# Kernel tuning notes

Hardware: AMD Instinct MI355X
Metric: run time of the kernel (lower is better)

The kernel has to match this reference:

```python
import jax, jax.numpy as jnp
import numpy as np


def _normalize_mat(AI):
    # symmetric GCN normalization: D^{-1/2} AI D^{-1/2}, safe for zero rows
    deg = jnp.sum(AI, axis=-1)  # [B, N]
    inv_sqrt = jnp.where(deg > 0, jax.lax.rsqrt(jnp.maximum(deg, 1e-12)), 0.0)
    return AI * inv_sqrt[..., :, None] * inv_sqrt[..., None, :]


def setup_inputs() -> dict:
    key = jax.random.key(0)
    kX, kA, kn, kW, kK = jax.random.split(key, 5)
    B, N, F, OUT, KD = 8, 2048, 256, 256, 32
    X = jax.random.normal(kX, (B, N, F), dtype=jnp.float32)
    A = jax.random.uniform(kA, (B, N, N), dtype=jnp.float32)
    A = 0.5 * (A + jnp.swapaxes(A, -1, -2))  # symmetric dense adjacency weights
    n = jax.random.randint(kn, (B,), 1, N + 1).astype(jnp.int32)
    W = jax.random.normal(kW, (F, OUT), dtype=jnp.float32) * (1.0 / np.sqrt(F))
    W_bias = jnp.zeros((OUT,), dtype=jnp.float32)
    K = jax.random.normal(kK, (F, KD), dtype=jnp.float32) * (1.0 / np.sqrt(F))
    K_bias = jnp.zeros((KD,), dtype=jnp.float32)
    return {"X": X, "A": A, "n": n, "W": W, "W_bias": W_bias, "K": K, "K_bias": K_bias}


def reference(X, A, n, W, W_bias, K, K_bias):
    B, N, F = X.shape
    Id = jnp.eye(N, dtype=X.dtype)  # broadcasts over batch
    # K-projection gating: sigmoid(XK @ XK^T) elementwise-masks A
    XK = jnp.einsum('bnf,fk->bnk', X, K) + K_bias  # [B, N, k_dim]
    A_filter = jax.nn.sigmoid(jnp.einsum('bik,bjk->bij', XK, XK))
    AI = A * A_filter + Id
    AI = _normalize_mat(AI)
    XW = jnp.einsum('bnf,fo->bno', X, W) + W_bias  # [B, N, out_dim]
    XWA = jnp.einsum('bij,bjo->bio', AI, XW)
    X_out = jax.nn.relu(XWA)
    return (X_out, A, n)
```

## Files before the change

kernel.cpp:

```cpp
#include <hip/hip_runtime.h>
#include <cstdint>
#include <cstddef>

#define Bz 8
#define Nn 2048
#define Ff 256
#define OUTD 256
#define KD 32

typedef __attribute__((ext_vector_type(8))) short bf16x8;
typedef __attribute__((ext_vector_type(4))) float f32x4;
typedef unsigned short ushort_t;

__device__ __forceinline__ ushort_t f2bf(float f) {
  union { float f; unsigned int u; } v; v.f = f;
  unsigned int r = v.u + 0x7FFFu + ((v.u >> 16) & 1u);
  return (ushort_t)(r >> 16);
}

__global__ __launch_bounds__(256) void k_xk(const float* __restrict__ X,
                                            const float* __restrict__ K,
                                            const float* __restrict__ Kb,
                                            ushort_t* __restrict__ XKbf) {
  int k = threadIdx.x & 31;
  int rl = threadIdx.x >> 5;
  int row = blockIdx.x * 8 + rl;
  const float* xr = X + (size_t)row * Ff;
  float acc = Kb[k];
#pragma unroll 8
  for (int f = 0; f < Ff; ++f) acc += xr[f] * K[f * KD + k];
  XKbf[(size_t)row * KD + k] = f2bf(acc);
}

__global__ __launch_bounds__(256) void k_degM(const float* __restrict__ A,
                                              const ushort_t* __restrict__ XKbf,
                                              ushort_t* __restrict__ M,
                                              float* __restrict__ deg) {
  int jt = blockIdx.x & 7;
  int it = (blockIdx.x >> 3) & 31;
  int b  = blockIdx.x >> 8;
  int i0 = it * 64, j0 = jt * 256;
  int tid = threadIdx.x;
  int lane = tid & 63, w = tid >> 6;
  int l15 = lane & 15, lh = lane >> 4;

  const ushort_t* XKb = XKbf + (size_t)b * Nn * KD;
  bf16x8 af[4], bfr[4];
#pragma unroll
  for (int m = 0; m < 4; ++m)
    af[m] = *(const bf16x8*)(XKb + (size_t)(i0 + 16 * m + l15) * KD + lh * 8);
#pragma unroll
  for (int n = 0; n < 4; ++n)
    bfr[n] = *(const bf16x8*)(XKb + (size_t)(j0 + 64 * w + 16 * n + l15) * KD + lh * 8);

  f32x4 S[4][4];
#pragma unroll
  for (int m = 0; m < 4; ++m)
#pragma unroll
    for (int n = 0; n < 4; ++n) {
      f32x4 z = {0.f, 0.f, 0.f, 0.f};
      S[m][n] = __builtin_amdgcn_mfma_f32_16x16x32_bf16(af[m], bfr[n], z, 0, 0, 0);
    }

  const float* Ab = A + (size_t)b * Nn * Nn;
  ushort_t* Mb = M + (size_t)b * Nn * Nn;
#pragma unroll
  for (int m = 0; m < 4; ++m) {
#pragma unroll
    for (int r = 0; r < 4; ++r) {
      int row = i0 + 16 * m + lh * 4 + r;
      float ds = 0.f;
#pragma unroll
      for (int n = 0; n < 4; ++n) {
        int col = j0 + 64 * w + 16 * n + l15;
        float d = S[m][n][r];
        float sg = 1.f / (1.f + __expf(-d));
        float mv = Ab[(size_t)row * Nn + col] * sg;
        Mb[(size_t)row * Nn + col] = f2bf(mv);
        ds += mv;
      }
      ds += __shfl_xor(ds, 1, 64);
      ds += __shfl_xor(ds, 2, 64);
      ds += __shfl_xor(ds, 4, 64);
      ds += __shfl_xor(ds, 8, 64);
      if (l15 == 0) atomicAdd(&deg[(size_t)b * Nn + row], ds);
    }
  }
}

__global__ __launch_bounds__(256) void k_xw(const float* __restrict__ X,
                                            const float* __restrict__ W,
                                            const float* __restrict__ Wb,
                                            const float* __restrict__ deg,
                                            float* __restrict__ XWs,
                                            ushort_t* __restrict__ XWsT) {
  __shared__ float Xs[8][Ff];
  int row0 = blockIdx.x * 8;
  int tid = threadIdx.x;
#pragma unroll
  for (int p = 0; p < 2; ++p) {
    int idx = tid + p * 256;
    int r = idx >> 6, c = (idx & 63) * 4;
    *(float4*)&Xs[r][c] = *(const float4*)(X + (size_t)(row0 + r) * Ff + c);
  }
  __syncthreads();
  int o = tid;
  float bias = Wb[o];
  float acc[8];
#pragma unroll
  for (int r = 0; r < 8; ++r) acc[r] = bias;
  for (int f = 0; f < Ff; ++f) {
    float w = W[f * OUTD + o];
#pragma unroll
    for (int r = 0; r < 8; ++r) acc[r] += Xs[r][f] * w;
  }
  int b = row0 / Nn;
  int rl0 = row0 - b * Nn;
  ushort_t mt[8];
#pragma unroll
  for (int r = 0; r < 8; ++r) {
    float is = rsqrtf(1.f + deg[row0 + r]);
    float v = acc[r] * is;
    XWs[(size_t)(row0 + r) * OUTD + o] = v;
    mt[r] = f2bf(v);
  }
  uint4 pk;
  pk.x = (unsigned)mt[0] | ((unsigned)mt[1] << 16);
  pk.y = (unsigned)mt[2] | ((unsigned)mt[3] << 16);
  pk.z = (unsigned)mt[4] | ((unsigned)mt[5] << 16);
  pk.w = (unsigned)mt[6] | ((unsigned)mt[7] << 16);
  *(uint4*)&XWsT[((size_t)b * OUTD + o) * Nn + rl0] = pk;
}

__device__ __forceinline__ void load6(const ushort_t* a0p, const ushort_t* a1p,
                                      const ushort_t* b0p, const ushort_t* b1p,
                                      const ushort_t* b2p, const ushort_t* b3p,
                                      int off,
                                      bf16x8& a0, bf16x8& a1,
                                      bf16x8& b0, bf16x8& b1, bf16x8& b2, bf16x8& b3) {
  a0 = *(const bf16x8*)(a0p + off);
  a1 = *(const bf16x8*)(a1p + off);
  b0 = *(const bf16x8*)(b0p + off);
  b1 = *(const bf16x8*)(b1p + off);
  b2 = *(const bf16x8*)(b2p + off);
  b3 = *(const bf16x8*)(b3p + off);
}

__device__ __forceinline__ void mm8(const bf16x8& a0, const bf16x8& a1,
                                    const bf16x8& b0, const bf16x8& b1,
                                    const bf16x8& b2, const bf16x8& b3,
                                    f32x4 acc[2][4]) {
  acc[0][0] = __builtin_amdgcn_mfma_f32_16x16x32_bf16(a0, b0, acc[0][0], 0, 0, 0);
  acc[0][1] = __builtin_amdgcn_mfma_f32_16x16x32_bf16(a0, b1, acc[0][1], 0, 0, 0);
  acc[0][2] = __builtin_amdgcn_mfma_f32_16x16x32_bf16(a0, b2, acc[0][2], 0, 0, 0);
  acc[0][3] = __builtin_amdgcn_mfma_f32_16x16x32_bf16(a0, b3, acc[0][3], 0, 0, 0);
  acc[1][0] = __builtin_amdgcn_mfma_f32_16x16x32_bf16(a1, b0, acc[1][0], 0, 0, 0);
  acc[1][1] = __builtin_amdgcn_mfma_f32_16x16x32_bf16(a1, b1, acc[1][1], 0, 0, 0);
  acc[1][2] = __builtin_amdgcn_mfma_f32_16x16x32_bf16(a1, b2, acc[1][2], 0, 0, 0);
  acc[1][3] = __builtin_amdgcn_mfma_f32_16x16x32_bf16(a1, b3, acc[1][3], 0, 0, 0);
}

__global__ __launch_bounds__(256) void k_main2(const ushort_t* __restrict__ M,
                                               const ushort_t* __restrict__ XWsT,
                                               const float* __restrict__ XWs,
                                               const float* __restrict__ deg,
                                               float* __restrict__ outX) {
  int it = blockIdx.x & 63;
  int b = blockIdx.x >> 6;
  int i0 = it * 32;
  int tid = threadIdx.x, lane = tid & 63, w = tid >> 6;
  int l15 = lane & 15, lh = lane >> 4;
  const ushort_t* Mb = M + (size_t)b * Nn * Nn;
  const ushort_t* Tb = XWsT + (size_t)b * OUTD * Nn;

  const ushort_t* a0p = Mb + (size_t)(i0 + l15) * Nn + lh * 8;
  const ushort_t* a1p = Mb + (size_t)(i0 + 16 + l15) * Nn + lh * 8;
  const ushort_t* b0p = Tb + (size_t)(64 * w + l15) * Nn + lh * 8;
  const ushort_t* b1p = Tb + (size_t)(64 * w + 16 + l15) * Nn + lh * 8;
  const ushort_t* b2p = Tb + (size_t)(64 * w + 32 + l15) * Nn + lh * 8;
  const ushort_t* b3p = Tb + (size_t)(64 * w + 48 + l15) * Nn + lh * 8;

  f32x4 acc[2][4];
#pragma unroll
  for (int m = 0; m < 2; ++m)
#pragma unroll
    for (int n = 0; n < 4; ++n) acc[m][n] = (f32x4){0.f, 0.f, 0.f, 0.f};

  bf16x8 aA0, aA1, bA0, bA1, bA2, bA3;
  bf16x8 aB0, aB1, bB0, bB1, bB2, bB3;
  bf16x8 aC0, aC1, bC0, bC1, bC2, bC3;
  bf16x8 aD0, aD1, bD0, bD1, bD2, bD3;

  load6(a0p, a1p, b0p, b1p, b2p, b3p, 0 * 32, aA0, aA1, bA0, bA1, bA2, bA3);
  load6(a0p, a1p, b0p, b1p, b2p, b3p, 1 * 32, aB0, aB1, bB0, bB1, bB2, bB3);
  load6(a0p, a1p, b0p, b1p, b2p, b3p, 2 * 32, aC0, aC1, bC0, bC1, bC2, bC3);
  load6(a0p, a1p, b0p, b1p, b2p, b3p, 3 * 32, aD0, aD1, bD0, bD1, bD2, bD3);

  for (int t = 0; t < 64; t += 4) {
    mm8(aA0, aA1, bA0, bA1, bA2, bA3, acc);
    if (t + 4 < 64) load6(a0p, a1p, b0p, b1p, b2p, b3p, (t + 4) * 32, aA0, aA1, bA0, bA1, bA2, bA3);
    mm8(aB0, aB1, bB0, bB1, bB2, bB3, acc);
    if (t + 5 < 64) load6(a0p, a1p, b0p, b1p, b2p, b3p, (t + 5) * 32, aB0, aB1, bB0, bB1, bB2, bB3);
    mm8(aC0, aC1, bC0, bC1, bC2, bC3, acc);
    if (t + 6 < 64) load6(a0p, a1p, b0p, b1p, b2p, b3p, (t + 6) * 32, aC0, aC1, bC0, bC1, bC2, bC3);
    mm8(aD0, aD1, bD0, bD1, bD2, bD3, acc);
    if (t + 7 < 64) load6(a0p, a1p, b0p, b1p, b2p, b3p, (t + 7) * 32, aD0, aD1, bD0, bD1, bD2, bD3);
  }

#pragma unroll
  for (int m = 0; m < 2; ++m) {
#pragma unroll
    for (int r = 0; r < 4; ++r) {
      int row = i0 + 16 * m + lh * 4 + r;
      float is = rsqrtf(1.f + deg[(size_t)b * Nn + row]);
#pragma unroll
      for (int n = 0; n < 4; ++n) {
        int col = 64 * w + 16 * n + l15;
        float v = acc[m][n][r] + XWs[((size_t)b * Nn + row) * OUTD + col];
        outX[((size_t)b * Nn + row) * OUTD + col] = fmaxf(0.f, is * v);
      }
    }
  }
}

__global__ void k_n(const int* __restrict__ n, float* __restrict__ o) {
  if (threadIdx.x < Bz) o[threadIdx.x] = (float)n[threadIdx.x];
}

extern "C" void kernel_launch(void* const* d_in, const int* in_sizes, int n_in,
                              void* d_out, int out_size, void* d_ws, size_t ws_size,
                              hipStream_t stream) {
  const float* X  = (const float*)d_in[0];
  const float* A  = (const float*)d_in[1];
  const int*   nI = (const int*)d_in[2];
  const float* W  = (const float*)d_in[3];
  const float* Wb = (const float*)d_in[4];
  const float* K  = (const float*)d_in[5];
  const float* Kb = (const float*)d_in[6];

  float* outX = (float*)d_out;
  float* outA = outX + (size_t)Bz * Nn * OUTD;
  float* outN = outA + (size_t)Bz * Nn * Nn;

  ushort_t* XKbf = (ushort_t*)d_ws;
  float* deg = (float*)(XKbf + (size_t)Bz * Nn * KD);
  float* XWs = deg + (size_t)Bz * Nn;
  ushort_t* XWsT = (ushort_t*)(XWs + (size_t)Bz * Nn * OUTD);

  ushort_t* Mws = (ushort_t*)outA;

  hipMemsetAsync(deg, 0, (size_t)Bz * Nn * sizeof(float), stream);
  k_xk  <<<dim3(Bz * Nn / 8),  dim3(256), 0, stream>>>(X, K, Kb, XKbf);
  k_degM<<<dim3(Bz * 32 * 8),  dim3(256), 0, stream>>>(A, XKbf, Mws, deg);
  k_xw  <<<dim3(Bz * Nn / 8),  dim3(256), 0, stream>>>(X, W, Wb, deg, XWs, XWsT);
  k_main2<<<dim3(Bz * 64),     dim3(256), 0, stream>>>(Mws, XWsT, XWs, deg, outX);

  hipMemcpyAsync(outA, A, (size_t)Bz * Nn * Nn * sizeof(float),
                 hipMemcpyDeviceToDevice, stream);
  k_n<<<1, 64, 0, stream>>>(nI, outN);
}
```

Before: 484.7 us.

## Fuse A passthrough copy into degM and stage main GEMM tiles through LDS

When the workspace is large enough, the bf16 M matrix goes into the workspace and k_degM writes the fp32 copy of A to the output as it reads it. This removes the separate device-to-device memcpy, which re-read all of A. The main aggregation kernel now stages M and XWsT tiles through double-buffered, XOR-swizzled shared memory, so a block's four waves share loads instead of each wave fetching its own operands from global memory. It also reorders block indices so the batch varies fastest. The fused path depends on ws_size, and the LDS version adds a barrier every k-step.

```diff
diff --git a/kernel.cpp b/kernel.cpp
--- a/kernel.cpp
+++ b/kernel.cpp
@@ -35,7 +35,8 @@
 __global__ __launch_bounds__(256) void k_degM(const float* __restrict__ A,
                                               const ushort_t* __restrict__ XKbf,
                                               ushort_t* __restrict__ M,
-                                              float* __restrict__ deg) {
+                                              float* __restrict__ deg,
+                                              float* __restrict__ Ao) {
   int jt = blockIdx.x & 7;
   int it = (blockIdx.x >> 3) & 31;
   int b  = blockIdx.x >> 8;
@@ -64,6 +65,7 @@
 
   const float* Ab = A + (size_t)b * Nn * Nn;
   ushort_t* Mb = M + (size_t)b * Nn * Nn;
+  float* Aob = Ao ? Ao + (size_t)b * Nn * Nn : nullptr;
 #pragma unroll
   for (int m = 0; m < 4; ++m) {
 #pragma unroll
@@ -73,9 +75,11 @@
 #pragma unroll
       for (int n = 0; n < 4; ++n) {
         int col = j0 + 64 * w + 16 * n + l15;
+        float a = Ab[(size_t)row * Nn + col];
+        if (Aob) Aob[(size_t)row * Nn + col] = a;
         float d = S[m][n][r];
         float sg = 1.f / (1.f + __expf(-d));
-        float mv = Ab[(size_t)row * Nn + col] * sg;
+        float mv = a * sg;
         Mb[(size_t)row * Nn + col] = f2bf(mv);
         ds += mv;
       }
@@ -132,79 +136,75 @@
   *(uint4*)&XWsT[((size_t)b * OUTD + o) * Nn + rl0] = pk;
 }
 
-__device__ __forceinline__ void load6(const ushort_t* a0p, const ushort_t* a1p,
-                                      const ushort_t* b0p, const ushort_t* b1p,
-                                      const ushort_t* b2p, const ushort_t* b3p,
-                                      int off,
-                                      bf16x8& a0, bf16x8& a1,
-                                      bf16x8& b0, bf16x8& b1, bf16x8& b2, bf16x8& b3) {
-  a0 = *(const bf16x8*)(a0p + off);
-  a1 = *(const bf16x8*)(a1p + off);
-  b0 = *(const bf16x8*)(b0p + off);
-  b1 = *(const bf16x8*)(b1p + off);
-  b2 = *(const bf16x8*)(b2p + off);
-  b3 = *(const bf16x8*)(b3p + off);
-}
-
-__device__ __forceinline__ void mm8(const bf16x8& a0, const bf16x8& a1,
-                                    const bf16x8& b0, const bf16x8& b1,
-                                    const bf16x8& b2, const bf16x8& b3,
-                                    f32x4 acc[2][4]) {
-  acc[0][0] = __builtin_amdgcn_mfma_f32_16x16x32_bf16(a0, b0, acc[0][0], 0, 0, 0);
-  acc[0][1] = __builtin_amdgcn_mfma_f32_16x16x32_bf16(a0, b1, acc[0][1], 0, 0, 0);
-  acc[0][2] = __builtin_amdgcn_mfma_f32_16x16x32_bf16(a0, b2, acc[0][2], 0, 0, 0);
-  acc[0][3] = __builtin_amdgcn_mfma_f32_16x16x32_bf16(a0, b3, acc[0][3], 0, 0, 0);
-  acc[1][0] = __builtin_amdgcn_mfma_f32_16x16x32_bf16(a1, b0, acc[1][0], 0, 0, 0);
-  acc[1][1] = __builtin_amdgcn_mfma_f32_16x16x32_bf16(a1, b1, acc[1][1], 0, 0, 0);
-  acc[1][2] = __builtin_amdgcn_mfma_f32_16x16x32_bf16(a1, b2, acc[1][2], 0, 0, 0);
-  acc[1][3] = __builtin_amdgcn_mfma_f32_16x16x32_bf16(a1, b3, acc[1][3], 0, 0, 0);
-}
-
-__global__ __launch_bounds__(256) void k_main2(const ushort_t* __restrict__ M,
+#define SWZB(row, grp16) ((unsigned)((row) * 64 + (((grp16) * 16) ^ (((row) & 7) << 4))))
+
+__global__ __launch_bounds__(256) void k_main3(const ushort_t* __restrict__ M,
                                                const ushort_t* __restrict__ XWsT,
                                                const float* __restrict__ XWs,
                                                const float* __restrict__ deg,
                                                float* __restrict__ outX) {
-  int it = blockIdx.x & 63;
-  int b = blockIdx.x >> 6;
-  int i0 = it * 32;
+  __shared__ __align__(16) ushort_t As[2][32 * 32];
+  __shared__ __align__(16) ushort_t Bs[2][256 * 32];
+  int b  = blockIdx.x & 7;
+  int i0 = (blockIdx.x >> 3) * 32;
   int tid = threadIdx.x, lane = tid & 63, w = tid >> 6;
   int l15 = lane & 15, lh = lane >> 4;
   const ushort_t* Mb = M + (size_t)b * Nn * Nn;
   const ushort_t* Tb = XWsT + (size_t)b * OUTD * Nn;
 
-  const ushort_t* a0p = Mb + (size_t)(i0 + l15) * Nn + lh * 8;
-  const ushort_t* a1p = Mb + (size_t)(i0 + 16 + l15) * Nn + lh * 8;
-  const ushort_t* b0p = Tb + (size_t)(64 * w + l15) * Nn + lh * 8;
-  const ushort_t* b1p = Tb + (size_t)(64 * w + 16 + l15) * Nn + lh * 8;
-  const ushort_t* b2p = Tb + (size_t)(64 * w + 32 + l15) * Nn + lh * 8;
-  const ushort_t* b3p = Tb + (size_t)(64 * w + 48 + l15) * Nn + lh * 8;
-
+  int r4 = tid >> 2;
+  int g3 = tid & 3;
+  const ushort_t* tb0 = Tb + (size_t)r4 * Nn + g3 * 8;
+  const ushort_t* mb0 = Mb + (size_t)(i0 + (r4 & 31)) * Nn + g3 * 8;
+
+  bf16x8 rB[4], rA;
   f32x4 acc[2][4];
 #pragma unroll
   for (int m = 0; m < 2; ++m)
 #pragma unroll
     for (int n = 0; n < 4; ++n) acc[m][n] = (f32x4){0.f, 0.f, 0.f, 0.f};
 
-  bf16x8 aA0, aA1, bA0, bA1, bA2, bA3;
-  bf16x8 aB0, aB1, bB0, bB1, bB2, bB3;
-  bf16x8 aC0, aC1, bC0, bC1, bC2, bC3;
-  bf16x8 aD0, aD1, bD0, bD1, bD2, bD3;
-
-  load6(a0p, a1p, b0p, b1p, b2p, b3p, 0 * 32, aA0, aA1, bA0, bA1, bA2, bA3);
-  load6(a0p, a1p, b0p, b1p, b2p, b3p, 1 * 32, aB0, aB1, bB0, bB1, bB2, bB3);
-  load6(a0p, a1p, b0p, b1p, b2p, b3p, 2 * 32, aC0, aC1, bC0, bC1, bC2, bC3);
-  load6(a0p, a1p, b0p, b1p, b2p, b3p, 3 * 32, aD0, aD1, bD0, bD1, bD2, bD3);
-
-  for (int t = 0; t < 64; t += 4) {
-    mm8(aA0, aA1, bA0, bA1, bA2, bA3, acc);
-    if (t + 4 < 64) load6(a0p, a1p, b0p, b1p, b2p, b3p, (t + 4) * 32, aA0, aA1, bA0, bA1, bA2, bA3);
-    mm8(aB0, aB1, bB0, bB1, bB2, bB3, acc);
-    if (t + 5 < 64) load6(a0p, a1p, b0p, b1p, b2p, b3p, (t + 5) * 32, aB0, aB1, bB0, bB1, bB2, bB3);
-    mm8(aC0, aC1, bC0, bC1, bC2, bC3, acc);
-    if (t + 6 < 64) load6(a0p, a1p, b0p, b1p, b2p, b3p, (t + 6) * 32, aC0, aC1, bC0, bC1, bC2, bC3);
-    mm8(aD0, aD1, bD0, bD1, bD2, bD3, acc);
-    if (t + 7 < 64) load6(a0p, a1p, b0p, b1p, b2p, b3p, (t + 7) * 32, aD0, aD1, bD0, bD1, bD2, bD3);
+#define LOAD_REGS(k0)                                                          \
+  {                                                                            \
+    _Pragma("unroll")                                                          \
+    for (int p = 0; p < 4; ++p)                                                \
+      rB[p] = *(const bf16x8*)(tb0 + (size_t)p * 64 * Nn + (k0));              \
+    if (tid < 128) rA = *(const bf16x8*)(mb0 + (k0));                          \
+  }
+
+#define WRITE_LDS(buf)                                                         \
+  {                                                                            \
+    _Pragma("unroll")                                                          \
+    for (int p = 0; p < 4; ++p)                                                \
+      *(bf16x8*)((char*)&Bs[buf][0] + SWZB(p * 64 + r4, g3)) = rB[p];          \
+    if (tid < 128) *(bf16x8*)((char*)&As[buf][0] + SWZB(r4, g3)) = rA;         \
+  }
+
+  LOAD_REGS(0);
+  WRITE_LDS(0);
+  __syncthreads();
+  LOAD_REGS(32);
+
+  int cur = 0;
+  for (int t = 0; t < 64; ++t) {
+    bf16x8 af0 = *(const bf16x8*)((char*)&As[cur][0] + SWZB(l15, lh));
+    bf16x8 af1 = *(const bf16x8*)((char*)&As[cur][0] + SWZB(16 + l15, lh));
+    bf16x8 bf0 = *(const bf16x8*)((char*)&Bs[cur][0] + SWZB(64 * w + l15, lh));
+    bf16x8 bf1 = *(const bf16x8*)((char*)&Bs[cur][0] + SWZB(64 * w + 16 + l15, lh));
+    bf16x8 bf2 = *(const bf16x8*)((char*)&Bs[cur][0] + SWZB(64 * w + 32 + l15, lh));
+    bf16x8 bf3 = *(const bf16x8*)((char*)&Bs[cur][0] + SWZB(64 * w + 48 + l15, lh));
+    acc[0][0] = __builtin_amdgcn_mfma_f32_16x16x32_bf16(af0, bf0, acc[0][0], 0, 0, 0);
+    acc[0][1] = __builtin_amdgcn_mfma_f32_16x16x32_bf16(af0, bf1, acc[0][1], 0, 0, 0);
+    acc[0][2] = __builtin_amdgcn_mfma_f32_16x16x32_bf16(af0, bf2, acc[0][2], 0, 0, 0);
+    acc[0][3] = __builtin_amdgcn_mfma_f32_16x16x32_bf16(af0, bf3, acc[0][3], 0, 0, 0);
+    acc[1][0] = __builtin_amdgcn_mfma_f32_16x16x32_bf16(af1, bf0, acc[1][0], 0, 0, 0);
+    acc[1][1] = __builtin_amdgcn_mfma_f32_16x16x32_bf16(af1, bf1, acc[1][1], 0, 0, 0);
+    acc[1][2] = __builtin_amdgcn_mfma_f32_16x16x32_bf16(af1, bf2, acc[1][2], 0, 0, 0);
+    acc[1][3] = __builtin_amdgcn_mfma_f32_16x16x32_bf16(af1, bf3, acc[1][3], 0, 0, 0);
+    if (t < 63) WRITE_LDS(cur ^ 1);
+    if (t < 62) LOAD_REGS((t + 2) * 32);
+    __syncthreads();
+    cur ^= 1;
   }
 
 #pragma unroll
@@ -246,16 +246,23 @@
   float* deg = (float*)(XKbf + (size_t)Bz * Nn * KD);
   float* XWs = deg + (size_t)Bz * Nn;
   ushort_t* XWsT = (ushort_t*)(XWs + (size_t)Bz * Nn * OUTD);
-
-  ushort_t* Mws = (ushort_t*)outA;
+  ushort_t* Mws_ws = XWsT + (size_t)Bz * OUTD * Nn;
+
+  const size_t need = (size_t)Bz * Nn * KD * 2 + (size_t)Bz * Nn * 4 +
+                      (size_t)Bz * Nn * OUTD * 4 + (size_t)Bz * OUTD * Nn * 2 +
+                      (size_t)Bz * Nn * Nn * 2;
+  bool fused = ws_size >= need;
+  ushort_t* Mp = fused ? Mws_ws : (ushort_t*)outA;
+  float* AoP  = fused ? outA : nullptr;
 
   hipMemsetAsync(deg, 0, (size_t)Bz * Nn * sizeof(float), stream);
-  k_xk  <<<dim3(Bz * Nn / 8),  dim3(256), 0, stream>>>(X, K, Kb, XKbf);
-  k_degM<<<dim3(Bz * 32 * 8),  dim3(256), 0, stream>>>(A, XKbf, Mws, deg);
-  k_xw  <<<dim3(Bz * Nn / 8),  dim3(256), 0, stream>>>(X, W, Wb, deg, XWs, XWsT);
-  k_main2<<<dim3(Bz * 64),     dim3(256), 0, stream>>>(Mws, XWsT, XWs, deg, outX);
-
-  hipMemcpyAsync(outA, A, (size_t)Bz * Nn * Nn * sizeof(float),
-                 hipMemcpyDeviceToDevice, stream);
+  k_xk  <<<dim3(Bz * Nn / 8), dim3(256), 0, stream>>>(X, K, Kb, XKbf);
+  k_degM<<<dim3(Bz * 32 * 8), dim3(256), 0, stream>>>(A, XKbf, Mp, deg, AoP);
+  k_xw  <<<dim3(Bz * Nn / 8), dim3(256), 0, stream>>>(X, W, Wb, deg, XWs, XWsT);
+  k_main3<<<dim3(Bz * 64),    dim3(256), 0, stream>>>(Mp, XWsT, XWs, deg, outX);
+  if (!fused) {
+    hipMemcpyAsync(outA, A, (size_t)Bz * Nn * Nn * sizeof(float),
+                   hipMemcpyDeviceToDevice, stream);
+  }
   k_n<<<1, 64, 0, stream>>>(nI, outN);
 }
```

New measurement: 467.6 us. -3.5%, faster.
